# Performance work log

Hardware: AMD Instinct MI355X
Metric: run time of the kernel (lower is better)

Reference implementation:

```python
import jax, jax.numpy as jnp
import numpy as np

N = 8192
EPS = 1e-12

def setup_inputs() -> dict:
    key = jax.random.key(0)
    k1, k2 = jax.random.split(key)
    var_1 = jax.random.normal(k1, (N,), dtype=jnp.float32)          # e.g. bb mass
    var_2 = jax.random.uniform(k2, (N,), dtype=jnp.float32)          # classifier output in (0,1)
    normedweight = jnp.ones((N,), dtype=jnp.float32)                 # weights sum to N
    return {"var_1": var_1, "var_2": var_2, "normedweight": normedweight, "power": 2}


def reference(var_1, var_2, normedweight, power):
    # Pairwise absolute difference matrices [N, N]
    amat = jnp.abs(var_1[:, None] - var_1[None, :])
    bmat = jnp.abs(var_2[:, None] - var_2[None, :])

    # Weighted row means (weight broadcasts along columns, mean over axis=1)
    amatavg = jnp.mean(amat * normedweight, axis=1)                  # [N]
    bmatavg = jnp.mean(bmat * normedweight, axis=1)                  # [N]

    # Double centering: minuend_1[i,j] = avg[j], minuend_2[i,j] = avg[i]
    Amat = amat - amatavg[None, :] - amatavg[:, None] + jnp.mean(amatavg * normedweight)
    Bmat = bmat - bmatavg[None, :] - bmatavg[:, None] + jnp.mean(bmatavg * normedweight)

    ABavg = jnp.abs(jnp.mean(Amat * Bmat * normedweight, axis=1))    # [N]
    AAavg = jnp.mean(Amat * Amat * normedweight, axis=1)             # [N]
    BBavg = jnp.mean(Bmat * Bmat * normedweight, axis=1)             # [N]

    num = jnp.mean(ABavg * normedweight)
    den = jnp.abs(jnp.mean(AAavg * normedweight) * jnp.mean(BBavg * normedweight))

    if power == 1:
        dCorr = num / jnp.sqrt(den + EPS)
    elif power == 2:
        dCorr = num ** 2 / (den + EPS)
    else:
        dCorr = (num / jnp.sqrt(jnp.mean(AAavg * normedweight) * jnp.mean(BBavg * normedweight)) + EPS) ** power

    # Original clamps NaN and negative results to 0
    dCorr = jnp.where(jnp.isnan(dCorr), jnp.float32(0.0), dCorr)
    dCorr = jnp.maximum(dCorr, jnp.float32(0.0))
    return dCorr
```

## Files before the change

kernel.cpp:

```cpp
#include <hip/hip_runtime.h>
#include <math.h>


#define NN 8192
#define BLK 256
#define RPT 4
#define ROWS_PER_BLOCK 16
#define GRIDX 512
#define CSPLIT 4
#define SEGC 2048
#define ITERS 8
#define MIDB 32

__device__ __forceinline__ void p1_elem(
    float aj, float bj, float wj,
    const float* __restrict__ ai, const float* __restrict__ bi,
    float* __restrict__ sa, float* __restrict__ sb) {
#pragma unroll
  for (int m = 0; m < RPT; ++m) {
    sa[m] = fmaf(fabsf(ai[m] - aj), wj, sa[m]);
    sb[m] = fmaf(fabsf(bi[m] - bj), wj, sb[m]);
  }
}

__device__ __forceinline__ void p2_elem(
    float aj, float bj, float wj, float avgaj, float avgbj,
    float ha, float hb,
    const float* __restrict__ ai, const float* __restrict__ bi,
    const float* __restrict__ ra, const float* __restrict__ rb,
    float* __restrict__ sAB, float* __restrict__ sAA, float* __restrict__ sBB) {
  const float caj = avgaj - ha;
  const float cbj = avgbj - hb;
#pragma unroll
  for (int m = 0; m < RPT; ++m) {
    const float A = (fabsf(ai[m] - aj) - ra[m]) - caj;
    const float B = (fabsf(bi[m] - bj) - rb[m]) - cbj;
    const float Aw = A * wj;
    const float Bw = B * wj;
    sAB[m] = fmaf(Aw, B, sAB[m]);
    sAA[m] = fmaf(Aw, A, sAA[m]);
    sBB[m] = fmaf(Bw, B, sBB[m]);
  }
}

__global__ __launch_bounds__(BLK) void k_pass1(
    const float* __restrict__ a, const float* __restrict__ b,
    const float* __restrict__ w,
    float* __restrict__ pa, float* __restrict__ pb) {
  const int lane = threadIdx.x & 63;
  const int wv = threadIdx.x >> 6;
  const int i0 = blockIdx.x * ROWS_PER_BLOCK + wv * RPT;
  const int seg = blockIdx.y;

  float ai[RPT], bi[RPT], sa[RPT], sb[RPT];
#pragma unroll
  for (int m = 0; m < RPT; ++m) {
    ai[m] = a[i0 + m]; bi[m] = b[i0 + m];
    sa[m] = 0.f; sb[m] = 0.f;
  }

  const int jb = seg * SEGC;
  const float4* a4 = (const float4*)(a + jb) + lane;
  const float4* b4 = (const float4*)(b + jb) + lane;
  const float4* w4 = (const float4*)(w + jb) + lane;

  float4 A0 = a4[0], B0 = b4[0], W0 = w4[0];
#pragma unroll 1
  for (int k = 0; k < ITERS - 1; ++k) {
    const int nx = (k + 1) * 64;
    const float4 A1 = a4[nx], B1 = b4[nx], W1 = w4[nx];
    p1_elem(A0.x, B0.x, W0.x, ai, bi, sa, sb);
    p1_elem(A0.y, B0.y, W0.y, ai, bi, sa, sb);
    p1_elem(A0.z, B0.z, W0.z, ai, bi, sa, sb);
    p1_elem(A0.w, B0.w, W0.w, ai, bi, sa, sb);
    A0 = A1; B0 = B1; W0 = W1;
  }
  p1_elem(A0.x, B0.x, W0.x, ai, bi, sa, sb);
  p1_elem(A0.y, B0.y, W0.y, ai, bi, sa, sb);
  p1_elem(A0.z, B0.z, W0.z, ai, bi, sa, sb);
  p1_elem(A0.w, B0.w, W0.w, ai, bi, sa, sb);

#pragma unroll
  for (int off = 32; off >= 1; off >>= 1) {
#pragma unroll
    for (int m = 0; m < RPT; ++m) {
      sa[m] += __shfl_xor(sa[m], off);
      sb[m] += __shfl_xor(sb[m], off);
    }
  }
  if (lane == 0) {
#pragma unroll
    for (int m = 0; m < RPT; ++m) {
      pa[seg * NN + i0 + m] = sa[m];
      pb[seg * NN + i0 + m] = sb[m];
    }
  }
}

__global__ __launch_bounds__(BLK) void k_mid(
    const float* __restrict__ pa, const float* __restrict__ pb,
    const float* __restrict__ w,
    float* __restrict__ avga, float* __restrict__ avgb,
    double* __restrict__ gA, double* __restrict__ gB) {
  const int i = blockIdx.x * BLK + threadIdx.x;
  const float av = (pa[i] + pa[NN + i] + pa[2 * NN + i] + pa[3 * NN + i]) * (1.0f / NN);
  const float bv = (pb[i] + pb[NN + i] + pb[2 * NN + i] + pb[3 * NN + i]) * (1.0f / NN);
  avga[i] = av; avgb[i] = bv;
  double sa = (double)av * (double)w[i];
  double sb = (double)bv * (double)w[i];
#pragma unroll
  for (int off = 32; off >= 1; off >>= 1) {
    sa += __shfl_xor(sa, off);
    sb += __shfl_xor(sb, off);
  }
  __shared__ double lsa[4], lsb[4];
  const int lane = threadIdx.x & 63;
  const int wv = threadIdx.x >> 6;
  if (lane == 0) { lsa[wv] = sa; lsb[wv] = sb; }
  __syncthreads();
  if (threadIdx.x == 0) {
    gA[blockIdx.x] = lsa[0] + lsa[1] + lsa[2] + lsa[3];
    gB[blockIdx.x] = lsb[0] + lsb[1] + lsb[2] + lsb[3];
  }
}

__global__ __launch_bounds__(BLK) void k_pass2(
    const float* __restrict__ a, const float* __restrict__ b,
    const float* __restrict__ w,
    const float* __restrict__ avga, const float* __restrict__ avgb,
    const double* __restrict__ gA, const double* __restrict__ gB,
    float* __restrict__ pAB, float* __restrict__ pAA, float* __restrict__ pBB) {
  const int lane = threadIdx.x & 63;
  const int wv = threadIdx.x >> 6;
  const int i0 = blockIdx.x * ROWS_PER_BLOCK + wv * RPT;
  const int seg = blockIdx.y;

  double da = gA[lane & (MIDB - 1)];
  double db = gB[lane & (MIDB - 1)];
#pragma unroll
  for (int off = 16; off >= 1; off >>= 1) {
    da += __shfl_xor(da, off);
    db += __shfl_xor(db, off);
  }
  const float ha = (float)(0.5 * da / NN);
  const float hb = (float)(0.5 * db / NN);

  float ai[RPT], bi[RPT], ra[RPT], rb[RPT];
  float sAB[RPT], sAA[RPT], sBB[RPT];
#pragma unroll
  for (int m = 0; m < RPT; ++m) {
    ai[m] = a[i0 + m]; bi[m] = b[i0 + m];
    ra[m] = avga[i0 + m] - ha;
    rb[m] = avgb[i0 + m] - hb;
    sAB[m] = 0.f; sAA[m] = 0.f; sBB[m] = 0.f;
  }

  const int jb = seg * SEGC;
  const float4* a4  = (const float4*)(a + jb)    + lane;
  const float4* b4  = (const float4*)(b + jb)    + lane;
  const float4* w4  = (const float4*)(w + jb)    + lane;
  const float4* ca4 = (const float4*)(avga + jb) + lane;
  const float4* cb4 = (const float4*)(avgb + jb) + lane;

  float4 A0 = a4[0], B0 = b4[0], W0 = w4[0], CA0 = ca4[0], CB0 = cb4[0];
#pragma unroll 1
  for (int k = 0; k < ITERS - 1; ++k) {
    const int nx = (k + 1) * 64;
    const float4 A1 = a4[nx], B1 = b4[nx], W1 = w4[nx], CA1 = ca4[nx], CB1 = cb4[nx];
    p2_elem(A0.x, B0.x, W0.x, CA0.x, CB0.x, ha, hb, ai, bi, ra, rb, sAB, sAA, sBB);
    p2_elem(A0.y, B0.y, W0.y, CA0.y, CB0.y, ha, hb, ai, bi, ra, rb, sAB, sAA, sBB);
    p2_elem(A0.z, B0.z, W0.z, CA0.z, CB0.z, ha, hb, ai, bi, ra, rb, sAB, sAA, sBB);
    p2_elem(A0.w, B0.w, W0.w, CA0.w, CB0.w, ha, hb, ai, bi, ra, rb, sAB, sAA, sBB);
    A0 = A1; B0 = B1; W0 = W1; CA0 = CA1; CB0 = CB1;
  }
  p2_elem(A0.x, B0.x, W0.x, CA0.x, CB0.x, ha, hb, ai, bi, ra, rb, sAB, sAA, sBB);
  p2_elem(A0.y, B0.y, W0.y, CA0.y, CB0.y, ha, hb, ai, bi, ra, rb, sAB, sAA, sBB);
  p2_elem(A0.z, B0.z, W0.z, CA0.z, CB0.z, ha, hb, ai, bi, ra, rb, sAB, sAA, sBB);
  p2_elem(A0.w, B0.w, W0.w, CA0.w, CB0.w, ha, hb, ai, bi, ra, rb, sAB, sAA, sBB);

#pragma unroll
  for (int off = 32; off >= 1; off >>= 1) {
#pragma unroll
    for (int m = 0; m < RPT; ++m) {
      sAB[m] += __shfl_xor(sAB[m], off);
      sAA[m] += __shfl_xor(sAA[m], off);
      sBB[m] += __shfl_xor(sBB[m], off);
    }
  }
  if (lane == 0) {
#pragma unroll
    for (int m = 0; m < RPT; ++m) {
      pAB[seg * NN + i0 + m] = sAB[m];
      pAA[seg * NN + i0 + m] = sAA[m];
      pBB[seg * NN + i0 + m] = sBB[m];
    }
  }
}

__global__ __launch_bounds__(BLK) void k_tail(
    const float* __restrict__ pAB, const float* __restrict__ pAA,
    const float* __restrict__ pBB, const float* __restrict__ w,
    double* __restrict__ fAB, double* __restrict__ fAA, double* __restrict__ fBB) {
  const int i = blockIdx.x * BLK + threadIdx.x;
  const float sab = pAB[i] + pAB[NN + i] + pAB[2 * NN + i] + pAB[3 * NN + i];
  const float saa = pAA[i] + pAA[NN + i] + pAA[2 * NN + i] + pAA[3 * NN + i];
  const float sbb = pBB[i] + pBB[NN + i] + pBB[2 * NN + i] + pBB[3 * NN + i];
  const float wi = w[i];
  double ab = (double)(fabsf(sab) * wi);
  double aa = (double)(saa * wi);
  double bb = (double)(sbb * wi);
#pragma unroll
  for (int off = 32; off >= 1; off >>= 1) {
    ab += __shfl_xor(ab, off);
    aa += __shfl_xor(aa, off);
    bb += __shfl_xor(bb, off);
  }
  __shared__ double l[3][4];
  const int lane = threadIdx.x & 63;
  const int wv = threadIdx.x >> 6;
  if (lane == 0) { l[0][wv] = ab; l[1][wv] = aa; l[2][wv] = bb; }
  __syncthreads();
  if (threadIdx.x == 0) {
    fAB[blockIdx.x] = l[0][0] + l[0][1] + l[0][2] + l[0][3];
    fAA[blockIdx.x] = l[1][0] + l[1][1] + l[1][2] + l[1][3];
    fBB[blockIdx.x] = l[2][0] + l[2][1] + l[2][2] + l[2][3];
  }
}

__global__ __launch_bounds__(64) void k_fin(
    const double* __restrict__ fAB, const double* __restrict__ fAA,
    const double* __restrict__ fBB, const int* __restrict__ powerPtr,
    float* __restrict__ out) {
  const int lane = threadIdx.x;
  double ab = fAB[lane & (MIDB - 1)];
  double aa = fAA[lane & (MIDB - 1)];
  double bb = fBB[lane & (MIDB - 1)];
#pragma unroll
  for (int off = 16; off >= 1; off >>= 1) {
    ab += __shfl_xor(ab, off);
    aa += __shfl_xor(aa, off);
    bb += __shfl_xor(bb, off);
  }
  if (lane == 0) {
    const double n2 = (double)NN * (double)NN;
    const double num = ab / n2;
    const double mAA = aa / n2;
    const double mBB = bb / n2;
    const double den = fabs(mAA * mBB);
    const int p = powerPtr[0];
    double d;
    if (p == 1) {
      d = num / sqrt(den + 1e-12);
    } else if (p == 2) {
      d = (num * num) / (den + 1e-12);
    } else {
      d = pow(num / sqrt(mAA * mBB) + 1e-12, (double)p);
    }
    if (isnan(d)) d = 0.0;
    if (d < 0.0) d = 0.0;
    out[0] = (float)d;
  }
}

extern "C" void kernel_launch(void* const* d_in, const int* in_sizes, int n_in,
                              void* d_out, int out_size, void* d_ws, size_t ws_size,
                              hipStream_t stream) {
  const float* a = (const float*)d_in[0];
  const float* b = (const float*)d_in[1];
  const float* w = (const float*)d_in[2];
  const int* power = (const int*)d_in[3];
  float* out = (float*)d_out;

  float* ws = (float*)d_ws;
  float* pa   = ws;
  float* pb   = pa + 4 * NN;
  float* pAB  = pb + 4 * NN;
  float* pAA  = pAB + 4 * NN;
  float* pBB  = pAA + 4 * NN;
  float* avga = pBB + 4 * NN;
  float* avgb = avga + NN;
  double* dbl = (double*)(avgb + NN);
  double* gA  = dbl;
  double* gB  = gA + MIDB;
  double* fAB = gB + MIDB;
  double* fAA = fAB + MIDB;
  double* fBB = fAA + MIDB;

  const dim3 grid(GRIDX, CSPLIT);
  k_pass1<<<grid, BLK, 0, stream>>>(a, b, w, pa, pb);
  k_mid<<<MIDB, BLK, 0, stream>>>(pa, pb, w, avga, avgb, gA, gB);
  k_pass2<<<grid, BLK, 0, stream>>>(a, b, w, avga, avgb, gA, gB, pAB, pAA, pBB);
  k_tail<<<MIDB, BLK, 0, stream>>>(pAB, pAA, pBB, w, fAB, fAA, fBB);
  k_fin<<<1, 64, 0, stream>>>(fAB, fAA, fBB, power, out);
}
```

Before: 43.31 us.

## Expand double-centered products algebraically into separable moments and partial sums

Pass 2 now accumulates five raw sums per row (w·|da|·|db|, and the r/s-weighted |da| and |db| terms). It no longer forms the centered A and B values per pair. The global mean correction is computed in pass1 and mid, and the centering terms are reassembled in k_tail from scalar moments in double precision. This removes the per-pair centering arithmetic and swaps the three squared-product accumulators for five FMA accumulators. The trade-offs are more partial-sum traffic, higher register pressure, and possible cancellation error in the expanded AA/BB formulas.

Result: slower. 45.48 us (+5.0%).

```diff
diff --git a/kernel.cpp b/kernel.cpp
--- a/kernel.cpp
+++ b/kernel.cpp
@@ -10,7 +10,9 @@
 #define CSPLIT 4
 #define SEGC 2048
 #define ITERS 8
+#define NBLK (GRIDX * CSPLIT)
 #define MIDB 32
+#define INV_N (1.0f / NN)
 
 __device__ __forceinline__ void p1_elem(
     float aj, float bj, float wj,
@@ -23,30 +25,11 @@
   }
 }
 
-__device__ __forceinline__ void p2_elem(
-    float aj, float bj, float wj, float avgaj, float avgbj,
-    float ha, float hb,
-    const float* __restrict__ ai, const float* __restrict__ bi,
-    const float* __restrict__ ra, const float* __restrict__ rb,
-    float* __restrict__ sAB, float* __restrict__ sAA, float* __restrict__ sBB) {
-  const float caj = avgaj - ha;
-  const float cbj = avgbj - hb;
-#pragma unroll
-  for (int m = 0; m < RPT; ++m) {
-    const float A = (fabsf(ai[m] - aj) - ra[m]) - caj;
-    const float B = (fabsf(bi[m] - bj) - rb[m]) - cbj;
-    const float Aw = A * wj;
-    const float Bw = B * wj;
-    sAB[m] = fmaf(Aw, B, sAB[m]);
-    sAA[m] = fmaf(Aw, A, sAA[m]);
-    sBB[m] = fmaf(Bw, B, sBB[m]);
-  }
-}
-
 __global__ __launch_bounds__(BLK) void k_pass1(
     const float* __restrict__ a, const float* __restrict__ b,
     const float* __restrict__ w,
-    float* __restrict__ pa, float* __restrict__ pb) {
+    float* __restrict__ pa, float* __restrict__ pb,
+    double* __restrict__ gpa, double* __restrict__ gpb) {
   const int lane = threadIdx.x & 63;
   const int wv = threadIdx.x >> 6;
   const int i0 = blockIdx.x * ROWS_PER_BLOCK + wv * RPT;
@@ -88,127 +71,209 @@
       sb[m] += __shfl_xor(sb[m], off);
     }
   }
+
+  __shared__ double gla[4], glb[4];
   if (lane == 0) {
 #pragma unroll
     for (int m = 0; m < RPT; ++m) {
       pa[seg * NN + i0 + m] = sa[m];
       pb[seg * NN + i0 + m] = sb[m];
     }
+    double da = 0.0, db = 0.0;
+#pragma unroll
+    for (int m = 0; m < RPT; ++m) {
+      const double wi = (double)w[i0 + m];
+      da += (double)sa[m] * wi;
+      db += (double)sb[m] * wi;
+    }
+    gla[wv] = da; glb[wv] = db;
+  }
+  __syncthreads();
+  if (threadIdx.x == 0) {
+    const int bid = blockIdx.y * GRIDX + blockIdx.x;
+    gpa[bid] = gla[0] + gla[1] + gla[2] + gla[3];
+    gpb[bid] = glb[0] + glb[1] + glb[2] + glb[3];
   }
 }
 
 __global__ __launch_bounds__(BLK) void k_mid(
+    const float* __restrict__ a, const float* __restrict__ b,
+    const float* __restrict__ w,
     const float* __restrict__ pa, const float* __restrict__ pb,
-    const float* __restrict__ w,
+    const double* __restrict__ gpa, const double* __restrict__ gpb,
     float* __restrict__ avga, float* __restrict__ avgb,
-    double* __restrict__ gA, double* __restrict__ gB) {
-  const int i = blockIdx.x * BLK + threadIdx.x;
-  const float av = (pa[i] + pa[NN + i] + pa[2 * NN + i] + pa[3 * NN + i]) * (1.0f / NN);
-  const float bv = (pb[i] + pb[NN + i] + pb[2 * NN + i] + pb[3 * NN + i]) * (1.0f / NN);
-  avga[i] = av; avgb[i] = bv;
-  double sa = (double)av * (double)w[i];
-  double sb = (double)bv * (double)w[i];
-#pragma unroll
-  for (int off = 32; off >= 1; off >>= 1) {
-    sa += __shfl_xor(sa, off);
-    sb += __shfl_xor(sb, off);
-  }
-  __shared__ double lsa[4], lsb[4];
+    float* __restrict__ rr, float* __restrict__ ss,
+    float* __restrict__ wr, float* __restrict__ ws,
+    double* __restrict__ scal) {
   const int lane = threadIdx.x & 63;
   const int wv = threadIdx.x >> 6;
-  if (lane == 0) { lsa[wv] = sa; lsb[wv] = sb; }
+
+  __shared__ double gsum[2];
+  if (wv < 2) {
+    const double* g = wv ? gpb : gpa;
+    double s = 0.0;
+    for (int k = 0; k < NBLK / 64; ++k) s += g[lane + 64 * k];
+#pragma unroll
+    for (int off = 32; off >= 1; off >>= 1) s += __shfl_xor(s, off);
+    if (lane == 0) gsum[wv] = s;
+  }
+  __syncthreads();
+  const float ha = (float)(0.5 * gsum[0] / ((double)NN * (double)NN));
+  const float hb = (float)(0.5 * gsum[1] / ((double)NN * (double)NN));
+
+  const int i = blockIdx.x * BLK + threadIdx.x;
+  const float av = (pa[i] + pa[NN + i] + pa[2 * NN + i] + pa[3 * NN + i]) * INV_N;
+  const float bv = (pb[i] + pb[NN + i] + pb[2 * NN + i] + pb[3 * NN + i]) * INV_N;
+  const float ri = av - ha;
+  const float si = bv - hb;
+  const float wi = w[i], aiv = a[i], biv = b[i];
+  avga[i] = av; avgb[i] = bv;
+  rr[i] = ri;  ss[i] = si;
+  wr[i] = wi * ri; ws[i] = wi * si;
+
+  double p[10];
+  p[0] = (double)wi;
+  p[1] = (double)wi * aiv;
+  p[2] = (double)wi * aiv * aiv;
+  p[3] = (double)wi * biv;
+  p[4] = (double)wi * biv * biv;
+  p[5] = (double)wi * ri;
+  p[6] = (double)wi * si;
+  p[7] = (double)wi * ri * ri;
+  p[8] = (double)wi * si * si;
+  p[9] = (double)wi * ri * si;
+#pragma unroll
+  for (int off = 32; off >= 1; off >>= 1) {
+#pragma unroll
+    for (int t = 0; t < 10; ++t) p[t] += __shfl_xor(p[t], off);
+  }
+  __shared__ double lp[10][4];
+  if (lane == 0) {
+#pragma unroll
+    for (int t = 0; t < 10; ++t) lp[t][wv] = p[t];
+  }
   __syncthreads();
   if (threadIdx.x == 0) {
-    gA[blockIdx.x] = lsa[0] + lsa[1] + lsa[2] + lsa[3];
-    gB[blockIdx.x] = lsb[0] + lsb[1] + lsb[2] + lsb[3];
+#pragma unroll
+    for (int t = 0; t < 10; ++t)
+      scal[t * MIDB + blockIdx.x] = lp[t][0] + lp[t][1] + lp[t][2] + lp[t][3];
   }
 }
 
 __global__ __launch_bounds__(BLK) void k_pass2(
     const float* __restrict__ a, const float* __restrict__ b,
     const float* __restrict__ w,
-    const float* __restrict__ avga, const float* __restrict__ avgb,
-    const double* __restrict__ gA, const double* __restrict__ gB,
-    float* __restrict__ pAB, float* __restrict__ pAA, float* __restrict__ pBB) {
+    const float* __restrict__ wr, const float* __restrict__ ws,
+    float* __restrict__ Qp, float* __restrict__ P1a, float* __restrict__ P2,
+    float* __restrict__ P3, float* __restrict__ P1b) {
   const int lane = threadIdx.x & 63;
   const int wv = threadIdx.x >> 6;
   const int i0 = blockIdx.x * ROWS_PER_BLOCK + wv * RPT;
   const int seg = blockIdx.y;
 
-  double da = gA[lane & (MIDB - 1)];
-  double db = gB[lane & (MIDB - 1)];
-#pragma unroll
-  for (int off = 16; off >= 1; off >>= 1) {
-    da += __shfl_xor(da, off);
-    db += __shfl_xor(db, off);
-  }
-  const float ha = (float)(0.5 * da / NN);
-  const float hb = (float)(0.5 * db / NN);
-
-  float ai[RPT], bi[RPT], ra[RPT], rb[RPT];
-  float sAB[RPT], sAA[RPT], sBB[RPT];
+  float ai[RPT], bi[RPT];
+  float q[RPT], g1a[RPT], g2[RPT], g3[RPT], g1b[RPT];
 #pragma unroll
   for (int m = 0; m < RPT; ++m) {
     ai[m] = a[i0 + m]; bi[m] = b[i0 + m];
-    ra[m] = avga[i0 + m] - ha;
-    rb[m] = avgb[i0 + m] - hb;
-    sAB[m] = 0.f; sAA[m] = 0.f; sBB[m] = 0.f;
+    q[m] = 0.f; g1a[m] = 0.f; g2[m] = 0.f; g3[m] = 0.f; g1b[m] = 0.f;
   }
 
   const int jb = seg * SEGC;
-  const float4* a4  = (const float4*)(a + jb)    + lane;
-  const float4* b4  = (const float4*)(b + jb)    + lane;
-  const float4* w4  = (const float4*)(w + jb)    + lane;
-  const float4* ca4 = (const float4*)(avga + jb) + lane;
-  const float4* cb4 = (const float4*)(avgb + jb) + lane;
-
-  float4 A0 = a4[0], B0 = b4[0], W0 = w4[0], CA0 = ca4[0], CB0 = cb4[0];
+  const float4* a4 = (const float4*)(a + jb)  + lane;
+  const float4* b4 = (const float4*)(b + jb)  + lane;
+  const float4* w4 = (const float4*)(w + jb)  + lane;
+  const float4* r4 = (const float4*)(wr + jb) + lane;
+  const float4* s4 = (const float4*)(ws + jb) + lane;
+
 #pragma unroll 1
-  for (int k = 0; k < ITERS - 1; ++k) {
-    const int nx = (k + 1) * 64;
-    const float4 A1 = a4[nx], B1 = b4[nx], W1 = w4[nx], CA1 = ca4[nx], CB1 = cb4[nx];
-    p2_elem(A0.x, B0.x, W0.x, CA0.x, CB0.x, ha, hb, ai, bi, ra, rb, sAB, sAA, sBB);
-    p2_elem(A0.y, B0.y, W0.y, CA0.y, CB0.y, ha, hb, ai, bi, ra, rb, sAB, sAA, sBB);
-    p2_elem(A0.z, B0.z, W0.z, CA0.z, CB0.z, ha, hb, ai, bi, ra, rb, sAB, sAA, sBB);
-    p2_elem(A0.w, B0.w, W0.w, CA0.w, CB0.w, ha, hb, ai, bi, ra, rb, sAB, sAA, sBB);
-    A0 = A1; B0 = B1; W0 = W1; CA0 = CA1; CB0 = CB1;
-  }
-  p2_elem(A0.x, B0.x, W0.x, CA0.x, CB0.x, ha, hb, ai, bi, ra, rb, sAB, sAA, sBB);
-  p2_elem(A0.y, B0.y, W0.y, CA0.y, CB0.y, ha, hb, ai, bi, ra, rb, sAB, sAA, sBB);
-  p2_elem(A0.z, B0.z, W0.z, CA0.z, CB0.z, ha, hb, ai, bi, ra, rb, sAB, sAA, sBB);
-  p2_elem(A0.w, B0.w, W0.w, CA0.w, CB0.w, ha, hb, ai, bi, ra, rb, sAB, sAA, sBB);
+  for (int k = 0; k < ITERS; ++k) {
+    const int ix = k * 64;
+    const float4 A = a4[ix], B = b4[ix], Wt = w4[ix], R = r4[ix], S = s4[ix];
+#define P2E(e)                                            \
+    {                                                     \
+      _Pragma("unroll")                                   \
+      for (int m = 0; m < RPT; ++m) {                     \
+        const float dd = fabsf(ai[m] - A.e);              \
+        const float ee = fabsf(bi[m] - B.e);              \
+        g1a[m] = fmaf(R.e, dd, g1a[m]);                   \
+        g2[m]  = fmaf(S.e, dd, g2[m]);                    \
+        g3[m]  = fmaf(R.e, ee, g3[m]);                    \
+        g1b[m] = fmaf(S.e, ee, g1b[m]);                   \
+        q[m]   = fmaf(Wt.e * dd, ee, q[m]);               \
+      }                                                   \
+    }
+    P2E(x) P2E(y) P2E(z) P2E(w)
+#undef P2E
+  }
 
 #pragma unroll
   for (int off = 32; off >= 1; off >>= 1) {
 #pragma unroll
     for (int m = 0; m < RPT; ++m) {
-      sAB[m] += __shfl_xor(sAB[m], off);
-      sAA[m] += __shfl_xor(sAA[m], off);
-      sBB[m] += __shfl_xor(sBB[m], off);
+      q[m]   += __shfl_xor(q[m], off);
+      g1a[m] += __shfl_xor(g1a[m], off);
+      g2[m]  += __shfl_xor(g2[m], off);
+      g3[m]  += __shfl_xor(g3[m], off);
+      g1b[m] += __shfl_xor(g1b[m], off);
     }
   }
   if (lane == 0) {
 #pragma unroll
     for (int m = 0; m < RPT; ++m) {
-      pAB[seg * NN + i0 + m] = sAB[m];
-      pAA[seg * NN + i0 + m] = sAA[m];
-      pBB[seg * NN + i0 + m] = sBB[m];
+      const int o = seg * NN + i0 + m;
+      Qp[o] = q[m]; P1a[o] = g1a[m]; P2[o] = g2[m];
+      P3[o] = g3[m]; P1b[o] = g1b[m];
     }
   }
 }
 
 __global__ __launch_bounds__(BLK) void k_tail(
-    const float* __restrict__ pAB, const float* __restrict__ pAA,
-    const float* __restrict__ pBB, const float* __restrict__ w,
+    const float* __restrict__ a, const float* __restrict__ b,
+    const float* __restrict__ w,
+    const float* __restrict__ avga, const float* __restrict__ avgb,
+    const float* __restrict__ rr, const float* __restrict__ ss,
+    const float* __restrict__ Qp, const float* __restrict__ P1a,
+    const float* __restrict__ P2, const float* __restrict__ P3,
+    const float* __restrict__ P1b,
+    const double* __restrict__ scal,
     double* __restrict__ fAB, double* __restrict__ fAA, double* __restrict__ fBB) {
+  const int lane = threadIdx.x & 63;
+  const int wv = threadIdx.x >> 6;
+
+  __shared__ double sc[10];
+  if (threadIdx.x < 10) {
+    double s = 0.0;
+    for (int k = 0; k < MIDB; ++k) s += scal[threadIdx.x * MIDB + k];
+    sc[threadIdx.x] = s;
+  }
+  __syncthreads();
+  const double W   = sc[0], Ma1 = sc[1], Ma2 = sc[2], Mb1 = sc[3], Mb2 = sc[4];
+  const double Swr = sc[5], Sws = sc[6], Swr2 = sc[7], Sws2 = sc[8], Swrs = sc[9];
+
   const int i = blockIdx.x * BLK + threadIdx.x;
-  const float sab = pAB[i] + pAB[NN + i] + pAB[2 * NN + i] + pAB[3 * NN + i];
-  const float saa = pAA[i] + pAA[NN + i] + pAA[2 * NN + i] + pAA[3 * NN + i];
-  const float sbb = pBB[i] + pBB[NN + i] + pBB[2 * NN + i] + pBB[3 * NN + i];
-  const float wi = w[i];
-  double ab = (double)(fabsf(sab) * wi);
-  double aa = (double)(saa * wi);
-  double bb = (double)(sbb * wi);
+  const double Qi   = (double)Qp[i]  + Qp[NN + i]  + Qp[2 * NN + i]  + Qp[3 * NN + i];
+  const double P1ai = (double)P1a[i] + P1a[NN + i] + P1a[2 * NN + i] + P1a[3 * NN + i];
+  const double P2i  = (double)P2[i]  + P2[NN + i]  + P2[2 * NN + i]  + P2[3 * NN + i];
+  const double P3i  = (double)P3[i]  + P3[NN + i]  + P3[2 * NN + i]  + P3[3 * NN + i];
+  const double P1bi = (double)P1b[i] + P1b[NN + i] + P1b[2 * NN + i] + P1b[3 * NN + i];
+  const double av = avga[i], bv = avgb[i], ri = rr[i], si = ss[i];
+  const double aiv = a[i], biv = b[i], wi = w[i];
+  const double P0a = av * (double)NN;
+  const double P0b = bv * (double)NN;
+
+  const double TAB = Qi - si * P0a - P2i - ri * P0b - P3i
+                   + ri * si * W + ri * Sws + si * Swr + Swrs;
+  const double TAA = (aiv * aiv * W - 2.0 * aiv * Ma1 + Ma2)
+                   - 2.0 * ri * P0a - 2.0 * P1ai
+                   + ri * ri * W + 2.0 * ri * Swr + Swr2;
+  const double TBB = (biv * biv * W - 2.0 * biv * Mb1 + Mb2)
+                   - 2.0 * si * P0b - 2.0 * P1bi
+                   + si * si * W + 2.0 * si * Sws + Sws2;
+
+  double ab = fabs(TAB) * wi;
+  double aa = TAA * wi;
+  double bb = TBB * wi;
 #pragma unroll
   for (int off = 32; off >= 1; off >>= 1) {
     ab += __shfl_xor(ab, off);
@@ -216,8 +281,6 @@
     bb += __shfl_xor(bb, off);
   }
   __shared__ double l[3][4];
-  const int lane = threadIdx.x & 63;
-  const int wv = threadIdx.x >> 6;
   if (lane == 0) { l[0][wv] = ab; l[1][wv] = aa; l[2][wv] = bb; }
   __syncthreads();
   if (threadIdx.x == 0) {
@@ -273,23 +336,31 @@
 
   float* ws = (float*)d_ws;
   float* pa   = ws;
-  float* pb   = pa + 4 * NN;
-  float* pAB  = pb + 4 * NN;
-  float* pAA  = pAB + 4 * NN;
-  float* pBB  = pAA + 4 * NN;
-  float* avga = pBB + 4 * NN;
+  float* pb   = pa  + 4 * NN;
+  float* Qp   = pb  + 4 * NN;
+  float* P1a  = Qp  + 4 * NN;
+  float* P2   = P1a + 4 * NN;
+  float* P3   = P2  + 4 * NN;
+  float* P1b  = P3  + 4 * NN;
+  float* avga = P1b + 4 * NN;
   float* avgb = avga + NN;
-  double* dbl = (double*)(avgb + NN);
-  double* gA  = dbl;
-  double* gB  = gA + MIDB;
-  double* fAB = gB + MIDB;
-  double* fAA = fAB + MIDB;
-  double* fBB = fAA + MIDB;
+  float* rr   = avgb + NN;
+  float* ss   = rr + NN;
+  float* wrv  = ss + NN;
+  float* wsv  = wrv + NN;
+  double* gpa  = (double*)(wsv + NN);
+  double* gpb  = gpa + NBLK;
+  double* scal = gpb + NBLK;
+  double* fAB  = scal + 10 * MIDB;
+  double* fAA  = fAB + MIDB;
+  double* fBB  = fAA + MIDB;
 
   const dim3 grid(GRIDX, CSPLIT);
-  k_pass1<<<grid, BLK, 0, stream>>>(a, b, w, pa, pb);
-  k_mid<<<MIDB, BLK, 0, stream>>>(pa, pb, w, avga, avgb, gA, gB);
-  k_pass2<<<grid, BLK, 0, stream>>>(a, b, w, avga, avgb, gA, gB, pAB, pAA, pBB);
-  k_tail<<<MIDB, BLK, 0, stream>>>(pAB, pAA, pBB, w, fAB, fAA, fBB);
+  k_pass1<<<grid, BLK, 0, stream>>>(a, b, w, pa, pb, gpa, gpb);
+  k_mid<<<MIDB, BLK, 0, stream>>>(a, b, w, pa, pb, gpa, gpb,
+                                  avga, avgb, rr, ss, wrv, wsv, scal);
+  k_pass2<<<grid, BLK, 0, stream>>>(a, b, w, wrv, wsv, Qp, P1a, P2, P3, P1b);
+  k_tail<<<MIDB, BLK, 0, stream>>>(a, b, w, avga, avgb, rr, ss,
+                                   Qp, P1a, P2, P3, P1b, scal, fAB, fAA, fBB);
   k_fin<<<1, 64, 0, stream>>>(fAB, fAA, fBB, power, out);
 }
```
